# Optimization experiments

Measured on AMD Instinct MI355X. Metric: run time of the kernel, lower is better.

## Reference

```python
import jax, jax.numpy as jnp
import numpy as np
import math

BS, L, NNF, NEF = 8, 107, 17, 9
NH, EH, H3, NL, K = 128, 32, 32, 10, 3
PC, TL, TH, FF, NCLS = 32, 3, 8, 256, 3
D = NH + PC
HD = D // TH
RPG = 150
N = BS * L
E = BS * (2 * (L - 1) + RPG)
EPS = 1e-5


def _ln(z, g, b):
    m = z.mean(-1, keepdims=True)
    v = ((z - m) ** 2).mean(-1, keepdims=True)
    return (z - m) / jnp.sqrt(v + EPS) * g + b


def _gelu(z):
    return jax.nn.gelu(z, approximate=False)


def _forward(x, edge_attr, cheb_w, cheb_b, ee_w, ee_b, mlp_w1, mlp_b1, mlp_w2, mlp_b2,
             root_w, conv_b, ln_g, ln_b, attn_in_w, attn_in_b, attn_out_w, attn_out_b,
             ff_w1, ff_b1, ff_w2, ff_b2, tln1_g, tln1_b, tln2_g, tln2_b, lin_w, lin_b,
             seq_edge_index, edge_index):
    n = x.shape[0]
    # --- ChebConv (K=3, sym norm, lambda_max=2 -> L_hat = -D^-1/2 A D^-1/2) on seq edges ---
    ss, sd = seq_edge_index[0], seq_edge_index[1]
    deg = jax.ops.segment_sum(jnp.ones_like(ss, dtype=x.dtype), ss, num_segments=n)
    dinv = jnp.where(deg > 0, jax.lax.rsqrt(jnp.maximum(deg, 1e-12)), 0.0)
    w = -(dinv[ss] * dinv[sd])
    lap = lambda h: jax.ops.segment_sum(w[:, None] * h[ss], sd, num_segments=n)
    tx1 = lap(x)
    tx2 = 2.0 * lap(tx1) - x
    h = x @ cheb_w[0] + tx1 @ cheb_w[1] + tx2 @ cheb_w[2] + cheb_b

    # --- edge encoder ---
    ea = edge_attr @ ee_w + ee_b
    src, dst = edge_index[0], edge_index[1]

    # --- NNConv: per-edge weight W_e = MLP(ea) in R^{NHxNH}; gather-matmul-scatter ---
    def nnconv(h, l):
        we = ((ea @ mlp_w1[l] + mlp_b1[l]) @ mlp_w2[l] + mlp_b2[l]).reshape(-1, NH, NH)
        msg = jnp.einsum('ei,eio->eo', h[src], we)
        return jax.ops.segment_sum(msg, dst, num_segments=n) + h @ root_w[l] + conv_b[l]

    h = nnconv(h, 0)  # layers[0].conv applied directly (no residual)
    for l in range(1, NL):  # DeepGCNLayer res+: x + conv(gelu(LN(x)))
        h = h + nnconv(_gelu(_ln(h, ln_g[l], ln_b[l])), l)
    h = _gelu(_ln(h, ln_g[0], ln_b[0]))  # reuses layer 0's norm/act

    # --- sinusoidal position encoding (dim=PC), concat ---
    p = jnp.arange(L, dtype=x.dtype)[:, None]
    div = jnp.exp(jnp.arange(0, PC, 2, dtype=x.dtype) * (-math.log(10000.0) / PC))
    pos = jnp.zeros((L, PC), dtype=x.dtype)
    pos = pos.at[:, 0::2].set(jnp.sin(p * div)).at[:, 1::2].set(jnp.cos(p * div))

    t = jnp.concatenate([h.reshape(BS, L, NH), jnp.broadcast_to(pos, (BS, L, PC))], -1)

    # --- post-norm TransformerEncoder (relu FFN), vectorized over graphs ---
    scale = 1.0 / math.sqrt(HD)
    for l in range(TL):
        qkv = t @ attn_in_w[l] + attn_in_b[l]
        q, k, v = jnp.split(qkv, 3, axis=-1)
        q = q.reshape(BS, L, TH, HD)
        k = k.reshape(BS, L, TH, HD)
        v = v.reshape(BS, L, TH, HD)
        a = jax.nn.softmax(jnp.einsum('bqhd,bkhd->bhqk', q, k) * scale, axis=-1)
        o = jnp.einsum('bhqk,bkhd->bqhd', a, v).reshape(BS, L, D) @ attn_out_w[l] + attn_out_b[l]
        t = _ln(t + o, tln1_g[l], tln1_b[l])
        f = jax.nn.relu(t @ ff_w1[l] + ff_b1[l]) @ ff_w2[l] + ff_b2[l]
        t = _ln(t + f, tln2_g[l], tln2_b[l])

    return t.reshape(n, D) @ lin_w + lin_b


def setup_inputs():
    rng = np.random.default_rng(0)
    ks = iter(jax.random.split(jax.random.key(0), 40))
    # bidirectional sequence edges per graph + random pair edges
    base = np.arange(L - 1)
    s = np.concatenate([base, base + 1])
    d = np.concatenate([base + 1, base])
    off = (np.arange(BS) * L)[:, None]
    seq_src = (s[None] + off).ravel()
    seq_dst = (d[None] + off).ravel()
    r_src = (rng.integers(0, L, (BS, RPG)) + off).ravel()
    r_dst = (rng.integers(0, L, (BS, RPG)) + off).ravel()
    edge_index = jnp.asarray(np.stack([np.concatenate([seq_src, r_src]),
                                       np.concatenate([seq_dst, r_dst])]), dtype=jnp.int32)
    seq_edge_index = jnp.asarray(np.stack([seq_src, seq_dst]), dtype=jnp.int32)
    n_seq = seq_src.shape[0]

    def nrm(shape, sc=0.05):
        return jax.random.normal(next(ks), shape, dtype=jnp.float32) * sc

    x = jax.random.normal(next(ks), (N, NNF), dtype=jnp.float32)
    edge_attr = jax.random.normal(next(ks), (E, NEF), dtype=jnp.float32)
    col0 = jnp.concatenate([jnp.zeros((n_seq,), jnp.float32), jnp.ones((E - n_seq,), jnp.float32)])
    edge_attr = edge_attr.at[:, 0].set(col0)
    return {
        'x': x, 'edge_attr': edge_attr,
        'cheb_w': nrm((K, NNF, NH), 0.1), 'cheb_b': nrm((NH,), 0.02),
        'ee_w': nrm((NEF, EH), 0.1), 'ee_b': nrm((EH,), 0.02),
        'mlp_w1': nrm((NL, EH, H3), 0.1), 'mlp_b1': nrm((NL, H3), 0.02),
        'mlp_w2': nrm((NL, H3, NH * NH), 0.01), 'mlp_b2': nrm((NL, NH * NH), 0.01),
        'root_w': nrm((NL, NH, NH), 0.05), 'conv_b': nrm((NL, NH), 0.02),
        'ln_g': jnp.ones((NL, NH), jnp.float32), 'ln_b': jnp.zeros((NL, NH), jnp.float32),
        'attn_in_w': nrm((TL, D, 3 * D), 0.05), 'attn_in_b': nrm((TL, 3 * D), 0.02),
        'attn_out_w': nrm((TL, D, D), 0.05), 'attn_out_b': nrm((TL, D), 0.02),
        'ff_w1': nrm((TL, D, FF), 0.05), 'ff_b1': nrm((TL, FF), 0.02),
        'ff_w2': nrm((TL, FF, D), 0.05), 'ff_b2': nrm((TL, D), 0.02),
        'tln1_g': jnp.ones((TL, D), jnp.float32), 'tln1_b': jnp.zeros((TL, D), jnp.float32),
        'tln2_g': jnp.ones((TL, D), jnp.float32), 'tln2_b': jnp.zeros((TL, D), jnp.float32),
        'lin_w': nrm((D, NCLS), 0.05), 'lin_b': nrm((NCLS,), 0.02),
        'seq_edge_index': seq_edge_index, 'edge_index': edge_index,
    }


def reference(x, edge_attr, cheb_w, cheb_b, ee_w, ee_b, mlp_w1, mlp_b1, mlp_w2, mlp_b2,
              root_w, conv_b, ln_g, ln_b, attn_in_w, attn_in_b, attn_out_w, attn_out_b,
              ff_w1, ff_b1, ff_w2, ff_b2, tln1_g, tln1_b, tln2_g, tln2_b, lin_w, lin_b,
              seq_edge_index, edge_index):
    return _forward(x, edge_attr, cheb_w, cheb_b, ee_w, ee_b, mlp_w1, mlp_b1, mlp_w2, mlp_b2,
                    root_w, conv_b, ln_g, ln_b, attn_in_w, attn_in_b, attn_out_w, attn_out_b,
                    ff_w1, ff_b1, ff_w2, ff_b2, tln1_g, tln1_b, tln2_g, tln2_b, lin_w, lin_b,
                    seq_edge_index, edge_index)
```

## Files before the change

### kernel.cpp

```cpp
#include <hip/hip_runtime.h>
#include <hip/hip_bf16.h>
#include <math.h>

#define BSZ   8
#define LSEQ  107
#define NNF   17
#define NEF   9
#define NH    128
#define EHD   32
#define H3D   32
#define NLAY  10
#define PCD   32
#define TLAY  3
#define THD   8
#define FFD   256
#define NCLS  3
#define DD    160
#define HDD   20
#define NND   856
#define NPAD  896
#define NE    2896
#define CSTR  32
#define QKVP  512
#define PRJP  192
#define KTOT  1408
#define ALD2  1416

#define SB_CHEB 428
#define SB_PAD  (SB_CHEB)
#define SB_CSR  (SB_PAD + 1)
#define NCSR    12
#define SB_TPK  (SB_CSR + NCSR)
#define NTPK    171
#define SB_BIAS (SB_TPK + NTPK)
#define SB_E10  (SB_BIAS + 1)
#define NE10    114
#define SB_WT   (SB_E10 + NE10)
#define NWT     160
#define SB_TOT  (SB_WT + NWT)

typedef __bf16 bf16;
typedef __bf16 bf16x8 __attribute__((ext_vector_type(8)));
typedef float  f32x4  __attribute__((ext_vector_type(4)));

__device__ __forceinline__ float geluf(float z) {
    return 0.5f * z * (1.0f + erff(z * 0.70710678118654752f));
}
__device__ __forceinline__ float wred(float v) {
    #pragma unroll
    for (int o = 32; o; o >>= 1) v += __shfl_xor(v, o, 64);
    return v;
}
__device__ __forceinline__ float dinv_path(int n) {
    return (n == 0 || n == LSEQ - 1) ? 1.0f : 0.70710678118654752f;
}

__global__ __launch_bounds__(256) void k_setup(
        const float* __restrict__ x, const float* __restrict__ cw,
        const float* __restrict__ cb, bf16* __restrict__ zA, bf16* __restrict__ zB,
        const float* __restrict__ eattr, const float* __restrict__ eew,
        const float* __restrict__ eeb, const float* __restrict__ w1,
        const float* __restrict__ b1,
        const float* __restrict__ w2, const float* __restrict__ b2,
        const float* __restrict__ rootw, bf16* __restrict__ bpk,
        float* __restrict__ e10,
        const int* __restrict__ ei, int* __restrict__ deg, int* __restrict__ csr,
        const float* __restrict__ ain_w, const float* __restrict__ aow,
        const float* __restrict__ ffw1, const float* __restrict__ ffw2,
        const float* __restrict__ ain_b, const float* __restrict__ aob,
        const float* __restrict__ ffb1, const float* __restrict__ ffb2,
        bf16* __restrict__ bqkv, bf16* __restrict__ bproj,
        bf16* __restrict__ bff1, bf16* __restrict__ bff2,
        float* __restrict__ tb_bias) {
    __shared__ __align__(16) char sm[24576];
    int blk = blockIdx.x, tid = threadIdx.x;
    if (blk < SB_CHEB) {
        float (*xs)[5][NNF] = (float (*)[5][NNF])sm;
        int s = tid >> 7, o = tid & 127;
        int n = blk * 2 + s;
        int g = n / LSEQ, i = n - g * LSEQ;
        if (o < 5 * NNF) {
            int k = o / NNF, f = o - k * NNF;
            int p = i - 2 + k; p = p < 0 ? 0 : (p > LSEQ - 1 ? LSEQ - 1 : p);
            xs[s][k][f] = x[(g * LSEQ + p) * NNF + f];
        }
        __syncthreads();
        float di  = dinv_path(i);
        float dm1 = dinv_path(i - 1 < 0 ? 0 : i - 1);
        float dp1 = dinv_path(i + 1 > LSEQ - 1 ? LSEQ - 1 : i + 1);
        float dm2 = dinv_path(i - 2 < 0 ? 0 : i - 2);
        float dp2 = dinv_path(i + 2 > LSEQ - 1 ? LSEQ - 1 : i + 2);
        float wmc = (i > 0)        ? -(dm1 * di) : 0.f;
        float wpc = (i < LSEQ - 1) ? -(dp1 * di) : 0.f;
        float wmm = (i - 1 > 0)        ? -(dm2 * dm1) : 0.f;
        float wpm = -(di * dm1);
        float wmp = -(di * dp1);
        float wpp = (i + 1 < LSEQ - 1) ? -(dp2 * dp1) : 0.f;
        float acc = cb[o];
        #pragma unroll
        for (int f = 0; f < NNF; ++f) {
            float xm2 = xs[s][0][f], xm1 = xs[s][1][f], x0 = xs[s][2][f],
                  xp1 = xs[s][3][f], xp2 = xs[s][4][f];
            float t1c = wmc * xm1 + wpc * xp1;
            float t1m = wmm * xm2 + wpm * x0;
            float t1p = wmp * x0 + wpp * xp2;
            float t2 = 2.f * (wmc * t1m + wpc * t1p) - x0;
            acc += x0 * cw[f * NH + o] + t1c * cw[(NNF + f) * NH + o]
                 + t2 * cw[(2 * NNF + f) * NH + o];
        }
        zA[n * NH + o] = (bf16)acc;
    } else if (blk == SB_PAD) {
        for (int i = tid; i < (NPAD - NND) * NH; i += 256) {
            zA[NND * NH + i] = (bf16)0.f;
            zB[NND * NH + i] = (bf16)0.f;
        }
    } else if (blk < SB_TPK) {
        int e = (blk - SB_CSR) * 256 + tid;
        if (e < NE) {
            int d = ei[NE + e];
            int slot = atomicAdd(&deg[d], 1);
            if (slot < CSTR) csr[d * CSTR + slot] = e;
        }
    } else if (blk < SB_BIAS) {
        bf16 (*tt)[65] = (bf16 (*)[65])sm;
        int v = blk - SB_TPK;
        int tl = v / 57, t = v % 57;
        const float* src; bf16* dst; int Kd, srcN, ct, kt;
        if (t < 24)      { ct = t & 7;  kt = t >> 3;          src = ain_w + (size_t)tl * DD * 3 * DD; srcN = 3 * DD; Kd = DD;  dst = bqkv  + (size_t)tl * QKVP * DD; }
        else if (t < 33) { int u = t - 24; ct = u % 3; kt = u / 3; src = aow + (size_t)tl * DD * DD;  srcN = DD;     Kd = DD;  dst = bproj + (size_t)tl * PRJP * DD; }
        else if (t < 45) { int u = t - 33; ct = u % 4; kt = u / 4; src = ffw1 + (size_t)tl * DD * FFD; srcN = FFD;   Kd = DD;  dst = bff1  + (size_t)tl * FFD * DD; }
        else             { int u = t - 45; ct = u % 3; kt = u / 3; src = ffw2 + (size_t)tl * FFD * DD; srcN = DD;    Kd = FFD; dst = bff2  + (size_t)tl * PRJP * FFD; }
        int cc = tid & 63, rr = tid >> 6;
        #pragma unroll
        for (int rep = 0; rep < 16; ++rep) {
            int kl = rep * 4 + rr;
            int k = kt * 64 + kl;
            int col = ct * 64 + cc;
            float val = (k < Kd && col < srcN) ? src[(size_t)k * srcN + col] : 0.f;
            tt[kl][cc] = (bf16)val;
        }
        __syncthreads();
        int k = kt * 64 + cc;
        if (k < Kd) {
            #pragma unroll
            for (int rep = 0; rep < 16; ++rep) {
                int c = rep * 4 + rr;
                dst[(size_t)(ct * 64 + c) * Kd + k] = tt[cc][c];
            }
        }
    } else if (blk == SB_BIAS) {
        for (int i = tid; i < 3 * 1152; i += 256) {
            int tl = i / 1152, r = i % 1152;
            float val;
            if (r < 512)      { val = (r < 480) ? ain_b[tl * 480 + r] : 0.f; }
            else if (r < 704) { int c = r - 512; val = (c < 160) ? aob[tl * 160 + c] : 0.f; }
            else if (r < 960) { int c = r - 704; val = ffb1[tl * 256 + c]; }
            else              { int c = r - 960; val = (c < 160) ? ffb2[tl * 160 + c] : 0.f; }
            tb_bias[i] = val;
        }
    } else if (blk < SB_WT) {
        int idx = (blk - SB_E10) * 256 + tid;
        if (idx < NE * 10) {
            int e = idx / 10, f = idx - e * 10;
            e10[idx] = (f < NEF) ? eattr[e * NEF + f] : 1.0f;
        }
    } else {
        float* gw  = (float*)sm;
        bf16* ldsT = (bf16*)(sm + 2048);
        int v = blk - SB_WT;
        int l = v >> 4, chunk = v & 15;
        int io0 = chunk * 1024;
        for (int e = tid; e < 320; e += 256) {
            int f = e >> 5, j = e & 31;
            float acc;
            if (f < 9) {
                acc = 0.f;
                for (int m = 0; m < EHD; ++m)
                    acc += eew[f * EHD + m] * w1[(size_t)l * EHD * H3D + m * H3D + j];
            } else {
                acc = b1[l * H3D + j];
                for (int m = 0; m < EHD; ++m)
                    acc += eeb[m] * w1[(size_t)l * EHD * H3D + m * H3D + j];
            }
            gw[e] = acc;
        }
        __syncthreads();
        int io = io0 + tid * 4;
        const float* w2l = w2 + (size_t)l * 524288;
        float acc[10][4];
        float4 b2v = *(const float4*)(b2 + (size_t)l * 16384 + io);
        #pragma unroll
        for (int f = 0; f < 9; ++f) { acc[f][0] = 0.f; acc[f][1] = 0.f; acc[f][2] = 0.f; acc[f][3] = 0.f; }
        acc[9][0] = b2v.x; acc[9][1] = b2v.y; acc[9][2] = b2v.z; acc[9][3] = b2v.w;
        for (int j = 0; j < H3D; ++j) {
            float4 wv4 = *(const float4*)(w2l + (size_t)j * 16384 + io);
            #pragma unroll
            for (int f = 0; f < 10; ++f) {
                float gf = gw[f * 32 + j];
                acc[f][0] += gf * wv4.x; acc[f][1] += gf * wv4.y;
                acc[f][2] += gf * wv4.z; acc[f][3] += gf * wv4.w;
            }
        }
        int o4 = (tid & 31) * 4, il = tid >> 5;
        #pragma unroll
        for (int f = 0; f < 10; ++f)
            #pragma unroll
            for (int k = 0; k < 4; ++k)
                ldsT[(f * 128 + o4 + k) * 8 + il] = (bf16)acc[f][k];
        float4 rv = *(const float4*)(rootw + (size_t)l * 16384 + io);
        ldsT[(10 * 128 + o4 + 0) * 8 + il] = (bf16)rv.x;
        ldsT[(10 * 128 + o4 + 1) * 8 + il] = (bf16)rv.y;
        ldsT[(10 * 128 + o4 + 2) * 8 + il] = (bf16)rv.z;
        ldsT[(10 * 128 + o4 + 3) * 8 + il] = (bf16)rv.w;
        __syncthreads();
        if (tid < 128) {
            int o = tid;
            bf16* dst = bpk + (size_t)l * 128 * KTOT + (size_t)o * KTOT + chunk * 8;
            #pragma unroll
            for (int f = 0; f < 11; ++f) {
                bf16x8 val = *(bf16x8*)(ldsT + ((size_t)f * 128 + o) * 8);
                *(bf16x8*)(dst + f * 128) = val;
            }
        }
    }
}

__global__ __launch_bounds__(256) void k_layer(const bf16* __restrict__ zin,
                                               float* __restrict__ h,
                                               const float* __restrict__ e10,
                                               const bf16* __restrict__ bpkL,
                                               const float* __restrict__ conv_b,
                                               const float* __restrict__ lng,
                                               const float* __restrict__ lnb,
                                               bf16* __restrict__ zout,
                                               float* __restrict__ tbuf,
                                               const int* __restrict__ ei,
                                               const int* __restrict__ deg,
                                               const int* __restrict__ csr,
                                               int l) {
    __shared__ bf16 As[16][ALD2];
    __shared__ float outs[16][128];
    int tid = threadIdx.x, lane = tid & 63, wv = tid >> 6;
    int r0 = blockIdx.x * 16;
    for (int rr = 0; rr < 4; ++rr) {
        int r = wv * 4 + rr;
        int d = r0 + r;
        float acc[10][2];
        #pragma unroll
        for (int f = 0; f < 10; ++f) { acc[f][0] = 0.f; acc[f][1] = 0.f; }
        int dg = 0;
        if (d < NND) { dg = deg[d]; if (dg > CSTR) dg = CSTR; }
        for (int k = 0; k < dg; ++k) {
            int e = csr[d * CSTR + k];
            int s = ei[e];
            float z0 = (float)zin[s * NH + lane];
            float z1 = (float)zin[s * NH + lane + 64];
            const float* ew = e10 + e * 10;
            #pragma unroll
            for (int f = 0; f < 10; ++f) {
                float wf = ew[f];
                acc[f][0] += wf * z0;
                acc[f][1] += wf * z1;
            }
        }
        #pragma unroll
        for (int f = 0; f < 10; ++f) {
            As[r][f * 128 + lane] = (bf16)acc[f][0];
            As[r][f * 128 + lane + 64] = (bf16)acc[f][1];
        }
        As[r][1280 + lane] = zin[d * NH + lane];
        As[r][1280 + lane + 64] = zin[d * NH + lane + 64];
    }
    __syncthreads();
    {
        int rA = lane & 15, q = lane >> 4, q8 = q * 8;
        const bf16* Af = &As[rA][0];
        int cb0 = wv * 32;
        const bf16* B0 = bpkL + (size_t)(cb0 + rA) * KTOT;
        const bf16* B1 = bpkL + (size_t)(cb0 + 16 + rA) * KTOT;
        f32x4 ac0 = {0.f, 0.f, 0.f, 0.f}, ac1 = ac0;
        for (int ks = 0; ks < KTOT / 32; ++ks) {
            int kb = ks * 32 + q8;
            bf16x8 av = *(const bf16x8*)(Af + kb);
            bf16x8 b0 = *(const bf16x8*)(B0 + kb);
            bf16x8 b1 = *(const bf16x8*)(B1 + kb);
            ac0 = __builtin_amdgcn_mfma_f32_16x16x32_bf16(av, b0, ac0, 0, 0, 0);
            ac1 = __builtin_amdgcn_mfma_f32_16x16x32_bf16(av, b1, ac1, 0, 0, 0);
        }
        #pragma unroll
        for (int reg = 0; reg < 4; ++reg) {
            outs[q * 4 + reg][cb0 + rA] = ac0[reg];
            outs[q * 4 + reg][cb0 + 16 + rA] = ac1[reg];
        }
    }
    __syncthreads();
    for (int rr = 0; rr < 4; ++rr) {
        int r = wv * 4 + rr;
        int d = r0 + r;
        if (d >= NND) {
            if (l < NLAY - 1) {
                zout[d * NH + lane] = (bf16)0.f;
                zout[d * NH + lane + 64] = (bf16)0.f;
            }
            continue;
        }
        float v0 = outs[r][lane] + conv_b[l * NH + lane];
        float v1 = outs[r][lane + 64] + conv_b[l * NH + lane + 64];
        if (l > 0) {
            v0 += h[d * NH + lane];
            v1 += h[d * NH + lane + 64];
        }
        if (l < NLAY - 1) {
            h[d * NH + lane] = v0;
            h[d * NH + lane + 64] = v1;
        }
        float m = wred(v0 + v1) * (1.f / NH);
        float d0 = v0 - m, d1 = v1 - m;
        float var = wred(d0 * d0 + d1 * d1) * (1.f / NH);
        float rs = rsqrtf(var + 1e-5f);
        if (l < NLAY - 1) {
            int ln = l + 1;
            zout[d * NH + lane] = (bf16)geluf(d0 * rs * lng[ln * NH + lane] + lnb[ln * NH + lane]);
            zout[d * NH + lane + 64] = (bf16)geluf(d1 * rs * lng[ln * NH + lane + 64] + lnb[ln * NH + lane + 64]);
        } else {
            tbuf[(size_t)d * DD + lane] = geluf(d0 * rs * lng[lane] + lnb[lane]);
            tbuf[(size_t)d * DD + lane + 64] = geluf(d1 * rs * lng[lane + 64] + lnb[lane + 64]);
        }
    }
    if (l == NLAY - 1) {
        for (int idx = tid; idx < 16 * PCD; idx += 256) {
            int r = idx >> 5, pc = idx & 31;
            int d = r0 + r;
            if (d < NND) {
                int qq = d % LSEQ;
                float twoi = (float)(pc & ~1);
                float ang = (float)qq * expf(-twoi * 0.28782313662425572f);
                tbuf[(size_t)d * DD + NH + pc] = (pc & 1) ? cosf(ang) : sinf(ang);
            }
        }
    }
}

__global__ __launch_bounds__(256) void k_gmm(const float* __restrict__ A,
                                             const bf16* __restrict__ bp,
                                             const float* __restrict__ biasP,
                                             float* __restrict__ C,
                                             int ksteps, int K, int PW, int act) {
    int lane = threadIdx.x & 63, wv = threadIdx.x >> 6;
    int m0 = blockIdx.y * 64 + wv * 16;
    int ct = blockIdx.x;
    int r = lane & 15, q = lane >> 4, q8 = q * 8;
    const float* Arow = A + (size_t)(m0 + r) * K;
    const bf16* Bb = bp + ((size_t)ct * 64 + r) * K;
    f32x4 a0 = {0.f,0.f,0.f,0.f}, a1 = a0, a2 = a0, a3 = a0;
    for (int ks = 0; ks < ksteps; ++ks) {
        int kb = ks * 32 + q8;
        float4 f0 = *(const float4*)(Arow + kb);
        float4 f1 = *(const float4*)(Arow + kb + 4);
        bf16x8 av;
        av[0] = (bf16)f0.x; av[1] = (bf16)f0.y; av[2] = (bf16)f0.z; av[3] = (bf16)f0.w;
        av[4] = (bf16)f1.x; av[5] = (bf16)f1.y; av[6] = (bf16)f1.z; av[7] = (bf16)f1.w;
        bf16x8 b0 = *(const bf16x8*)(Bb + 0 * 16 * K + kb);
        bf16x8 b1 = *(const bf16x8*)(Bb + 1 * 16 * K + kb);
        bf16x8 b2 = *(const bf16x8*)(Bb + 2 * 16 * K + kb);
        bf16x8 b3 = *(const bf16x8*)(Bb + 3 * 16 * K + kb);
        a0 = __builtin_amdgcn_mfma_f32_16x16x32_bf16(av, b0, a0, 0, 0, 0);
        a1 = __builtin_amdgcn_mfma_f32_16x16x32_bf16(av, b1, a1, 0, 0, 0);
        a2 = __builtin_amdgcn_mfma_f32_16x16x32_bf16(av, b2, a2, 0, 0, 0);
        a3 = __builtin_amdgcn_mfma_f32_16x16x32_bf16(av, b3, a3, 0, 0, 0);
    }
    int cb = ct * 64;
    #pragma unroll
    for (int reg = 0; reg < 4; ++reg) {
        float* Crow = C + (size_t)(m0 + q * 4 + reg) * PW + cb;
        float v0 = a0[reg] + biasP[cb + 0 * 16 + r];
        float v1 = a1[reg] + biasP[cb + 1 * 16 + r];
        float v2 = a2[reg] + biasP[cb + 2 * 16 + r];
        float v3 = a3[reg] + biasP[cb + 3 * 16 + r];
        if (act) { v0 = fmaxf(v0, 0.f); v1 = fmaxf(v1, 0.f); v2 = fmaxf(v2, 0.f); v3 = fmaxf(v3, 0.f); }
        Crow[0 * 16 + r] = v0;
        Crow[1 * 16 + r] = v1;
        Crow[2 * 16 + r] = v2;
        Crow[3 * 16 + r] = v3;
    }
}

__global__ __launch_bounds__(256) void k_pln(const float* __restrict__ A,
                                             const bf16* __restrict__ bp,
                                             const float* __restrict__ biasP,
                                             float* __restrict__ t,
                                             const float* __restrict__ g,
                                             const float* __restrict__ bvec,
                                             int ksteps, int K,
                                             const float* __restrict__ lw,
                                             const float* __restrict__ lb,
                                             float* __restrict__ outp) {
    __shared__ float outs[16][PRJP];
    int tid = threadIdx.x, lane = tid & 63, wv = tid >> 6;
    int m0 = blockIdx.x * 16;
    if (wv < 3) {
        int r = lane & 15, q = lane >> 4, q8 = q * 8;
        const float* Arow = A + (size_t)(m0 + r) * K;
        const bf16* Bb = bp + ((size_t)wv * 64 + r) * K;
        f32x4 a0 = {0.f,0.f,0.f,0.f}, a1 = a0, a2 = a0, a3 = a0;
        for (int ks = 0; ks < ksteps; ++ks) {
            int kb = ks * 32 + q8;
            float4 f0 = *(const float4*)(Arow + kb);
            float4 f1 = *(const float4*)(Arow + kb + 4);
            bf16x8 av;
            av[0] = (bf16)f0.x; av[1] = (bf16)f0.y; av[2] = (bf16)f0.z; av[3] = (bf16)f0.w;
            av[4] = (bf16)f1.x; av[5] = (bf16)f1.y; av[6] = (bf16)f1.z; av[7] = (bf16)f1.w;
            bf16x8 b0 = *(const bf16x8*)(Bb + 0 * 16 * K + kb);
            bf16x8 b1 = *(const bf16x8*)(Bb + 1 * 16 * K + kb);
            bf16x8 b2 = *(const bf16x8*)(Bb + 2 * 16 * K + kb);
            bf16x8 b3 = *(const bf16x8*)(Bb + 3 * 16 * K + kb);
            a0 = __builtin_amdgcn_mfma_f32_16x16x32_bf16(av, b0, a0, 0, 0, 0);
            a1 = __builtin_amdgcn_mfma_f32_16x16x32_bf16(av, b1, a1, 0, 0, 0);
            a2 = __builtin_amdgcn_mfma_f32_16x16x32_bf16(av, b2, a2, 0, 0, 0);
            a3 = __builtin_amdgcn_mfma_f32_16x16x32_bf16(av, b3, a3, 0, 0, 0);
        }
        int cb = wv * 64;
        #pragma unroll
        for (int reg = 0; reg < 4; ++reg) {
            int rw = q * 4 + reg;
            outs[rw][cb + 0 * 16 + r] = a0[reg] + biasP[cb + 0 * 16 + r];
            outs[rw][cb + 1 * 16 + r] = a1[reg] + biasP[cb + 1 * 16 + r];
            outs[rw][cb + 2 * 16 + r] = a2[reg] + biasP[cb + 2 * 16 + r];
            outs[rw][cb + 3 * 16 + r] = a3[reg] + biasP[cb + 3 * 16 + r];
        }
    }
    __syncthreads();
    for (int rr = 0; rr < 4; ++rr) {
        int r = wv * 4 + rr;
        int d = m0 + r;
        if (d >= NND) continue;
        int c0 = lane, c1 = lane + 64, c2 = lane + 128;
        float v0 = outs[r][c0] + t[(size_t)d * DD + c0];
        float v1 = outs[r][c1] + t[(size_t)d * DD + c1];
        float v2 = (lane < 32) ? (outs[r][c2] + t[(size_t)d * DD + c2]) : 0.f;
        float m = wred(v0 + v1 + v2) * (1.f / DD);
        float d0 = v0 - m, d1 = v1 - m, d2 = (lane < 32) ? (v2 - m) : 0.f;
        float var = wred(d0 * d0 + d1 * d1 + d2 * d2) * (1.f / DD);
        float rs = rsqrtf(var + 1e-5f);
        float n0 = d0 * rs * g[c0] + bvec[c0];
        float n1 = d1 * rs * g[c1] + bvec[c1];
        float n2 = (lane < 32) ? (d2 * rs * g[c2] + bvec[c2]) : 0.f;
        t[(size_t)d * DD + c0] = n0;
        t[(size_t)d * DD + c1] = n1;
        if (lane < 32) t[(size_t)d * DD + c2] = n2;
        if (outp) {
            #pragma unroll
            for (int cls = 0; cls < NCLS; ++cls) {
                float part = n0 * lw[c0 * NCLS + cls] + n1 * lw[c1 * NCLS + cls]
                           + ((lane < 32) ? n2 * lw[c2 * NCLS + cls] : 0.f);
                float tot = wred(part);
                if (lane == 0) outp[d * NCLS + cls] = tot + lb[cls];
            }
        }
    }
}

#define UPD4(ac, V) { ac.x = ac.x * corr + p * V.x; ac.y = ac.y * corr + p * V.y; \
                      ac.z = ac.z * corr + p * V.z; ac.w = ac.w * corr + p * V.w; }
__global__ __launch_bounds__(64) void k_attn(const float* __restrict__ qkv,
                                             float* __restrict__ aout) {
    __shared__ float4 Ks4[LSEQ * 5], Vs4[LSEQ * 5];
    int bh = blockIdx.x;
    int b = bh >> 3, hh = bh & 7;
    int tid = threadIdx.x;
    for (int i = tid; i < LSEQ * 5; i += 64) {
        int kq = i / 5, c4 = i - kq * 5;
        const float* rowp = qkv + (size_t)(b * LSEQ + kq) * QKVP + hh * HDD;
        Ks4[i] = ((const float4*)(rowp + DD))[c4];
        Vs4[i] = ((const float4*)(rowp + 2 * DD))[c4];
    }
    __syncthreads();
    int q = blockIdx.y * 64 + tid;
    if (q >= LSEQ) return;
    const float4* qp = (const float4*)(qkv + (size_t)(b * LSEQ + q) * QKVP + hh * HDD);
    float4 q0 = qp[0], q1 = qp[1], q2 = qp[2], q3 = qp[3], q4 = qp[4];
    const float scale = 0.22360679774997896f;
    float mx = -3.0e38f, sum = 0.f;
    float4 z = {0.f, 0.f, 0.f, 0.f};
    float4 ac0 = z, ac1 = z, ac2 = z, ac3 = z, ac4 = z;
    for (int k = 0; k < LSEQ; ++k) {
        const float4* kp = Ks4 + k * 5;
        float4 K0 = kp[0], K1 = kp[1], K2 = kp[2], K3 = kp[3], K4 = kp[4];
        float a0 = q0.x * K0.x + q0.y * K0.y + q0.z * K0.z + q0.w * K0.w;
        float a1 = q1.x * K1.x + q1.y * K1.y + q1.z * K1.z + q1.w * K1.w;
        float a2 = q2.x * K2.x + q2.y * K2.y + q2.z * K2.z + q2.w * K2.w;
        float a3 = q3.x * K3.x + q3.y * K3.y + q3.z * K3.z + q3.w * K3.w;
        float a4 = q4.x * K4.x + q4.y * K4.y + q4.z * K4.z + q4.w * K4.w;
        float s = (((a0 + a1) + (a2 + a3)) + a4) * scale;
        float mn = fmaxf(mx, s);
        float corr = __expf(mx - mn);
        float p = __expf(s - mn);
        mx = mn;
        sum = sum * corr + p;
        const float4* vp = Vs4 + k * 5;
        float4 V0 = vp[0], V1 = vp[1], V2 = vp[2], V3 = vp[3], V4 = vp[4];
        UPD4(ac0, V0); UPD4(ac1, V1); UPD4(ac2, V2); UPD4(ac3, V3); UPD4(ac4, V4);
    }
    float inv = 1.f / sum;
    float4* op = (float4*)(aout + (size_t)(b * LSEQ + q) * DD + hh * HDD);
    float4 o0 = {ac0.x * inv, ac0.y * inv, ac0.z * inv, ac0.w * inv};
    float4 o1 = {ac1.x * inv, ac1.y * inv, ac1.z * inv, ac1.w * inv};
    float4 o2 = {ac2.x * inv, ac2.y * inv, ac2.z * inv, ac2.w * inv};
    float4 o3 = {ac3.x * inv, ac3.y * inv, ac3.z * inv, ac3.w * inv};
    float4 o4 = {ac4.x * inv, ac4.y * inv, ac4.z * inv, ac4.w * inv};
    op[0] = o0; op[1] = o1; op[2] = o2; op[3] = o3; op[4] = o4;
}

extern "C" void kernel_launch(void* const* d_in, const int* in_sizes, int n_in,
                              void* d_out, int out_size, void* d_ws, size_t ws_size,
                              hipStream_t stream) {
    (void)in_sizes; (void)n_in; (void)out_size; (void)ws_size;
    const float* x      = (const float*)d_in[0];
    const float* eattr  = (const float*)d_in[1];
    const float* cheb_w = (const float*)d_in[2];
    const float* cheb_b = (const float*)d_in[3];
    const float* ee_w   = (const float*)d_in[4];
    const float* ee_b   = (const float*)d_in[5];
    const float* mlp_w1 = (const float*)d_in[6];
    const float* mlp_b1 = (const float*)d_in[7];
    const float* mlp_w2 = (const float*)d_in[8];
    const float* mlp_b2 = (const float*)d_in[9];
    const float* root_w = (const float*)d_in[10];
    const float* conv_b = (const float*)d_in[11];
    const float* ln_g   = (const float*)d_in[12];
    const float* ln_b   = (const float*)d_in[13];
    const float* ain_w  = (const float*)d_in[14];
    const float* ain_b  = (const float*)d_in[15];
    const float* aow    = (const float*)d_in[16];
    const float* aob    = (const float*)d_in[17];
    const float* ffw1   = (const float*)d_in[18];
    const float* ffb1   = (const float*)d_in[19];
    const float* ffw2   = (const float*)d_in[20];
    const float* ffb2   = (const float*)d_in[21];
    const float* t1g    = (const float*)d_in[22];
    const float* t1b    = (const float*)d_in[23];
    const float* t2g    = (const float*)d_in[24];
    const float* t2b    = (const float*)d_in[25];
    const float* lin_w  = (const float*)d_in[26];
    const float* lin_b  = (const float*)d_in[27];
    const int* ei       = (const int*)d_in[29];

    char* w = (char*)d_ws;
    size_t off = 0;
    auto alloc = [&](size_t bytes) -> void* {
        void* p = w + off;
        off += (bytes + 255) & ~(size_t)255;
        return p;
    };
    bf16*  bpk   = (bf16*)alloc((size_t)NLAY * 128 * KTOT * 2);
    float* e10   = (float*)alloc((size_t)NE * 10 * 4);
    float* h     = (float*)alloc((size_t)NND * NH * 4);
    bf16*  zA    = (bf16*)alloc((size_t)NPAD * NH * 2);
    bf16*  zB    = (bf16*)alloc((size_t)NPAD * NH * 2);
    float* tbuf  = (float*)alloc((size_t)NPAD * DD * 4);
    float* qkvC  = (float*)alloc((size_t)NPAD * QKVP * 4);
    float* abuf  = (float*)alloc((size_t)NPAD * DD * 4);
    float* f1    = (float*)alloc((size_t)NPAD * FFD * 4);
    int*   deg   = (int*)alloc((size_t)NND * 4);
    int*   csr   = (int*)alloc((size_t)NND * CSTR * 4);
    bf16*  bqkv  = (bf16*)alloc((size_t)TLAY * QKVP * DD * 2);
    bf16*  bproj = (bf16*)alloc((size_t)TLAY * PRJP * DD * 2);
    bf16*  bff1  = (bf16*)alloc((size_t)TLAY * FFD * DD * 2);
    bf16*  bff2  = (bf16*)alloc((size_t)TLAY * PRJP * FFD * 2);
    float* tbias = (float*)alloc((size_t)TLAY * 1152 * 4);

    hipMemsetAsync(deg, 0, (size_t)NND * 4, stream);

    k_setup<<<SB_TOT, 256, 0, stream>>>(x, cheb_w, cheb_b, zA, zB,
                                        eattr, ee_w, ee_b, mlp_w1, mlp_b1,
                                        mlp_w2, mlp_b2, root_w, bpk, e10,
                                        ei, deg, csr,
                                        ain_w, aow, ffw1, ffw2,
                                        ain_b, aob, ffb1, ffb2,
                                        bqkv, bproj, bff1, bff2, tbias);

    bf16* zcur = zA;
    bf16* znxt = zB;
    for (int l = 0; l < NLAY; ++l) {
        k_layer<<<NPAD / 16, 256, 0, stream>>>(zcur, h, e10, bpk + (size_t)l * 128 * KTOT,
                                               conv_b, ln_g, ln_b, znxt, tbuf,
                                               ei, deg, csr, l);
        bf16* tmp = zcur; zcur = znxt; znxt = tmp;
    }

    for (int tl = 0; tl < TLAY; ++tl) {
        const float* bb = tbias + (size_t)tl * 1152;
        k_gmm<<<dim3(QKVP / 64, 14), 256, 0, stream>>>(tbuf, bqkv + (size_t)tl * QKVP * DD,
                                                       bb, qkvC, 5, DD, QKVP, 0);
        k_attn<<<dim3(BSZ * THD, 2), 64, 0, stream>>>(qkvC, abuf);
        k_pln<<<NPAD / 16, 256, 0, stream>>>(abuf, bproj + (size_t)tl * PRJP * DD,
                                             bb + 512, tbuf,
                                             t1g + (size_t)tl * DD, t1b + (size_t)tl * DD,
                                             5, DD, nullptr, nullptr, nullptr);
        k_gmm<<<dim3(FFD / 64, 14), 256, 0, stream>>>(tbuf, bff1 + (size_t)tl * FFD * DD,
                                                      bb + 704, f1, 5, DD, FFD, 1);
        int last = (tl == TLAY - 1);
        k_pln<<<NPAD / 16, 256, 0, stream>>>(f1, bff2 + (size_t)tl * PRJP * FFD,
                                             bb + 960, tbuf,
                                             t2g + (size_t)tl * DD, t2b + (size_t)tl * DD,
                                             8, FFD,
                                             last ? lin_w : nullptr,
                                             last ? lin_b : nullptr,
                                             last ? (float*)d_out : nullptr);
    }
}
```

Before: 547.1 us.

## Fuse next-layer GEMM into projection+LayerNorm kernel and build CSR in one block

The post-LayerNorm output of each k_pln block is cached as bf16 in shared memory and immediately multiplied by the next weight matrix (FF1 after attention projection, next layer's QKV after FF2). This drops the separate k_gmm launches and the reload of tbuf from global memory. CSR construction now runs in a single setup block using shared-memory atomics and writes deg at the end, which removes the hipMemsetAsync. The trade-off is more work and shared memory per k_pln block, and a serialized CSR build inside setup.

```diff
diff --git a/kernel.cpp b/kernel.cpp
--- a/kernel.cpp
+++ b/kernel.cpp
@@ -28,9 +28,8 @@
 
 #define SB_CHEB 428
 #define SB_PAD  (SB_CHEB)
-#define SB_CSR  (SB_PAD + 1)
-#define NCSR    12
-#define SB_TPK  (SB_CSR + NCSR)
+#define SB_CSR1 (SB_PAD + 1)
+#define SB_TPK  (SB_CSR1 + 1)
 #define NTPK    171
 #define SB_BIAS (SB_TPK + NTPK)
 #define SB_E10  (SB_BIAS + 1)
@@ -114,13 +113,17 @@
             zA[NND * NH + i] = (bf16)0.f;
             zB[NND * NH + i] = (bf16)0.f;
         }
-    } else if (blk < SB_TPK) {
-        int e = (blk - SB_CSR) * 256 + tid;
-        if (e < NE) {
+    } else if (blk == SB_CSR1) {
+        int* ldeg = (int*)sm;
+        for (int i = tid; i < NND; i += 256) ldeg[i] = 0;
+        __syncthreads();
+        for (int e = tid; e < NE; e += 256) {
             int d = ei[NE + e];
-            int slot = atomicAdd(&deg[d], 1);
+            int slot = atomicAdd(&ldeg[d], 1);
             if (slot < CSTR) csr[d * CSTR + slot] = e;
         }
+        __syncthreads();
+        for (int i = tid; i < NND; i += 256) deg[i] = ldeg[i];
     } else if (blk < SB_BIAS) {
         bf16 (*tt)[65] = (bf16 (*)[65])sm;
         int v = blk - SB_TPK;
@@ -388,14 +391,19 @@
 __global__ __launch_bounds__(256) void k_pln(const float* __restrict__ A,
                                              const bf16* __restrict__ bp,
                                              const float* __restrict__ biasP,
+                                             int ksteps, int K,
                                              float* __restrict__ t,
                                              const float* __restrict__ g,
                                              const float* __restrict__ bvec,
-                                             int ksteps, int K,
+                                             int tail,
+                                             const bf16* __restrict__ tbp,
+                                             const float* __restrict__ tbias_,
+                                             float* __restrict__ tout,
                                              const float* __restrict__ lw,
                                              const float* __restrict__ lb,
                                              float* __restrict__ outp) {
     __shared__ float outs[16][PRJP];
+    __shared__ bf16 Als[16][176];
     int tid = threadIdx.x, lane = tid & 63, wv = tid >> 6;
     int m0 = blockIdx.x * 16;
     if (wv < 3) {
@@ -448,13 +456,54 @@
         t[(size_t)d * DD + c0] = n0;
         t[(size_t)d * DD + c1] = n1;
         if (lane < 32) t[(size_t)d * DD + c2] = n2;
-        if (outp) {
+        Als[r][c0] = (bf16)n0;
+        Als[r][c1] = (bf16)n1;
+        if (lane < 32) Als[r][c2] = (bf16)n2;
+        if (tail == 0 && outp) {
             #pragma unroll
             for (int cls = 0; cls < NCLS; ++cls) {
                 float part = n0 * lw[c0 * NCLS + cls] + n1 * lw[c1 * NCLS + cls]
                            + ((lane < 32) ? n2 * lw[c2 * NCLS + cls] : 0.f);
                 float tot = wred(part);
                 if (lane == 0) outp[d * NCLS + cls] = tot + lb[cls];
+            }
+        }
+    }
+    if (!tail) return;
+    __syncthreads();
+    {
+        int PW = (tail == 1) ? FFD : QKVP;
+        int ntile = (tail == 1) ? 1 : 2;
+        int rA = lane & 15, q = lane >> 4, q8 = q * 8;
+        for (int ctl = 0; ctl < ntile; ++ctl) {
+            int cb = (ctl * 4 + wv) * 64;
+            const bf16* Bb = tbp + ((size_t)cb + rA) * DD;
+            f32x4 a0 = {0.f,0.f,0.f,0.f}, a1 = a0, a2 = a0, a3 = a0;
+            #pragma unroll
+            for (int ks = 0; ks < 5; ++ks) {
+                int kb = ks * 32 + q8;
+                bf16x8 av = *(const bf16x8*)(&Als[rA][0] + kb);
+                bf16x8 b0 = *(const bf16x8*)(Bb + 0 * 16 * DD + kb);
+                bf16x8 b1 = *(const bf16x8*)(Bb + 1 * 16 * DD + kb);
+                bf16x8 b2 = *(const bf16x8*)(Bb + 2 * 16 * DD + kb);
+                bf16x8 b3 = *(const bf16x8*)(Bb + 3 * 16 * DD + kb);
+                a0 = __builtin_amdgcn_mfma_f32_16x16x32_bf16(av, b0, a0, 0, 0, 0);
+                a1 = __builtin_amdgcn_mfma_f32_16x16x32_bf16(av, b1, a1, 0, 0, 0);
+                a2 = __builtin_amdgcn_mfma_f32_16x16x32_bf16(av, b2, a2, 0, 0, 0);
+                a3 = __builtin_amdgcn_mfma_f32_16x16x32_bf16(av, b3, a3, 0, 0, 0);
+            }
+            #pragma unroll
+            for (int reg = 0; reg < 4; ++reg) {
+                float* Crow = tout + (size_t)(m0 + q * 4 + reg) * PW + cb;
+                float v0 = a0[reg] + tbias_[cb + 0 * 16 + rA];
+                float v1 = a1[reg] + tbias_[cb + 1 * 16 + rA];
+                float v2 = a2[reg] + tbias_[cb + 2 * 16 + rA];
+                float v3 = a3[reg] + tbias_[cb + 3 * 16 + rA];
+                if (tail == 1) { v0 = fmaxf(v0, 0.f); v1 = fmaxf(v1, 0.f); v2 = fmaxf(v2, 0.f); v3 = fmaxf(v3, 0.f); }
+                Crow[0 * 16 + rA] = v0;
+                Crow[1 * 16 + rA] = v1;
+                Crow[2 * 16 + rA] = v2;
+                Crow[3 * 16 + rA] = v3;
             }
         }
     }
@@ -569,8 +618,6 @@
     bf16*  bff2  = (bf16*)alloc((size_t)TLAY * PRJP * FFD * 2);
     float* tbias = (float*)alloc((size_t)TLAY * 1152 * 4);
 
-    hipMemsetAsync(deg, 0, (size_t)NND * 4, stream);
-
     k_setup<<<SB_TOT, 256, 0, stream>>>(x, cheb_w, cheb_b, zA, zB,
                                         eattr, ee_w, ee_b, mlp_w1, mlp_b1,
                                         mlp_w2, mlp_b2, root_w, bpk, e10,
@@ -588,22 +635,23 @@
         bf16* tmp = zcur; zcur = znxt; znxt = tmp;
     }
 
+    k_gmm<<<dim3(QKVP / 64, 14), 256, 0, stream>>>(tbuf, bqkv, tbias, qkvC, 5, DD, QKVP, 0);
     for (int tl = 0; tl < TLAY; ++tl) {
         const float* bb = tbias + (size_t)tl * 1152;
-        k_gmm<<<dim3(QKVP / 64, 14), 256, 0, stream>>>(tbuf, bqkv + (size_t)tl * QKVP * DD,
-                                                       bb, qkvC, 5, DD, QKVP, 0);
         k_attn<<<dim3(BSZ * THD, 2), 64, 0, stream>>>(qkvC, abuf);
-        k_pln<<<NPAD / 16, 256, 0, stream>>>(abuf, bproj + (size_t)tl * PRJP * DD,
-                                             bb + 512, tbuf,
+        k_pln<<<NPAD / 16, 256, 0, stream>>>(abuf, bproj + (size_t)tl * PRJP * DD, bb + 512,
+                                             5, DD, tbuf,
                                              t1g + (size_t)tl * DD, t1b + (size_t)tl * DD,
-                                             5, DD, nullptr, nullptr, nullptr);
-        k_gmm<<<dim3(FFD / 64, 14), 256, 0, stream>>>(tbuf, bff1 + (size_t)tl * FFD * DD,
-                                                      bb + 704, f1, 5, DD, FFD, 1);
+                                             1, bff1 + (size_t)tl * FFD * DD, bb + 704, f1,
+                                             nullptr, nullptr, nullptr);
         int last = (tl == TLAY - 1);
-        k_pln<<<NPAD / 16, 256, 0, stream>>>(f1, bff2 + (size_t)tl * PRJP * FFD,
-                                             bb + 960, tbuf,
+        k_pln<<<NPAD / 16, 256, 0, stream>>>(f1, bff2 + (size_t)tl * PRJP * FFD, bb + 960,
+                                             8, FFD, tbuf,
                                              t2g + (size_t)tl * DD, t2b + (size_t)tl * DD,
-                                             8, FFD,
+                                             last ? 0 : 2,
+                                             last ? nullptr : bqkv + (size_t)(tl + 1) * QKVP * DD,
+                                             last ? nullptr : tbias + (size_t)(tl + 1) * 1152,
+                                             last ? nullptr : qkvC,
                                              last ? lin_w : nullptr,
                                              last ? lin_b : nullptr,
                                              last ? (float*)d_out : nullptr);
```

Result: no change. 538.8 us (-1.5%).
